# Optimization experiments

Hardware: AMD Instinct MI355X
Metric: run time of the kernel (lower is better)

Reference implementation:

```python
import jax, jax.numpy as jnp
import numpy as np
from functools import reduce

IN_CH = 1; OUT_CH = 16; K = 3; PAD = 1; QDEPTH = 2; WIRES = 4; DIM = 2 ** WIRES

# --- precomputed CNOT permutation matrices (constants) ---
# PennyLane convention: wire 0 is the most significant bit of the basis index.
def _cnot_mat(control, target):
    perm = np.arange(DIM)
    cbit = 1 << (WIRES - 1 - control)
    tbit = 1 << (WIRES - 1 - target)
    flip = (perm & cbit).astype(bool)
    perm = np.where(flip, perm ^ tbit, perm)
    return jnp.asarray(np.eye(DIM, dtype=np.complex64)[perm])

# StronglyEntanglingLayers default ranges: r_l = l % (n_wires - 1) + 1
_CNOTS = [[_cnot_mat(i, (i + (l % (WIRES - 1) + 1)) % WIRES) for i in range(WIRES)]
          for l in range(QDEPTH)]

def _rot(angles):
    # qml.Rot(phi, theta, omega) = RZ(omega) @ RY(theta) @ RZ(phi)
    phi, theta, omega = angles[0], angles[1], angles[2]
    c = jnp.cos(theta / 2); s = jnp.sin(theta / 2)
    return jnp.stack([
        jnp.exp(-0.5j * (phi + omega)) * c, -jnp.exp(0.5j * (phi - omega)) * s,
        jnp.exp(-0.5j * (phi - omega)) * s,  jnp.exp(0.5j * (phi + omega)) * c,
    ]).reshape(2, 2)

def _sel_unitary(weights):
    # Full 16x16 unitary of StronglyEntanglingLayers(weights) -- dim is tiny,
    # so building the dense unitary once and batching patches through it is
    # the efficient form (vs. per-gate contractions over 2.1M state vectors).
    U = jnp.eye(DIM, dtype=jnp.complex64)
    for l in range(QDEPTH):
        layer = reduce(jnp.kron, [_rot(weights[l, i]) for i in range(WIRES)])
        U = layer @ U
        for C in _CNOTS[l]:
            U = C @ U
    return U

def setup_inputs() -> dict:
    key = jax.random.key(0)
    k1, k2 = jax.random.split(key)
    x = jax.random.normal(k1, (32, 1, 256, 256), dtype=jnp.float32)
    weights = jax.random.uniform(k2, (QDEPTH, WIRES, 3), dtype=jnp.float32)
    return {"x": x, "weights": weights}

def reference(x, weights):
    b, c, h_in, w_in = x.shape
    h_out = h_in + 2 * PAD - K + 1
    w_out = w_in + 2 * PAD - K + 1
    # ConstantPad2d with value 0.01
    xp = jnp.pad(x, ((0, 0), (0, 0), (PAD, PAD), (PAD, PAD)), constant_values=0.01)
    # unfold -> (b, c*K*K, h_out, w_out), feature order (c, k0, k1)
    patches = jax.lax.conv_general_dilated_patches(xp, (K, K), (1, 1), 'VALID')
    patches = patches.transpose(0, 2, 3, 1).reshape(b * h_out * w_out, K * K)
    # zero-pad patch vectors from K*K=9 to 2^wires=16, then L2-normalize (eps=1e-12)
    patches = jnp.pad(patches, ((0, 0), (0, DIM - K * K)))
    norm = jnp.linalg.norm(patches, axis=-1, keepdims=True)
    patches = patches / jnp.maximum(norm, 1e-12)
    # Mottonen prep on |0> yields the normalized patch exactly (up to global
    # phase); then apply the entangling-layer unitary and measure probs.
    state = patches.astype(jnp.complex64) @ _sel_unitary(weights).T  # (N, 16)
    probs = jnp.abs(state) ** 2
    out = jnp.clip(probs * (DIM * 0.5), 0.0, 1.0)[:, :OUT_CH]
    return out.reshape(b, h_out, w_out, OUT_CH).transpose(0, 3, 1, 2)
```

## Files before the change

kernel.cpp:

```cpp
#include <hip/hip_runtime.h>
#include <math.h>


#define WIRES 4
#define DIM 16

__device__ inline void rot_entry(float phi, float th, float om, int rb, int cb,
                                 float& er, float& ei) {
    float a = 0.5f * (phi + om);
    float b = 0.5f * (phi - om);
    float cc = cosf(0.5f * th), ss = sinf(0.5f * th);
    if (rb == 0 && cb == 0) { er = cc * cosf(a); ei = -cc * sinf(a); }
    else if (rb == 0 && cb == 1) { er = -ss * cosf(b); ei = -ss * sinf(b); }
    else if (rb == 1 && cb == 0) { er = ss * cosf(b); ei = -ss * sinf(b); }
    else { er = cc * cosf(a); ei = cc * sinf(a); }
}

__device__ inline void layer_elem(const float* __restrict__ w, int l, int r,
                                  int c, float& pr, float& pi) {
    pr = 1.f; pi = 0.f;
    #pragma unroll
    for (int i = 0; i < WIRES; ++i) {
        const float* wi = w + (l * WIRES + i) * 3;
        float er, ei;
        int rb = (r >> (3 - i)) & 1, cb = (c >> (3 - i)) & 1;
        rot_entry(wi[0], wi[1], wi[2], rb, cb, er, ei);
        float nr = pr * er - pi * ei;
        float ni = pr * ei + pi * er;
        pr = nr; pi = ni;
    }
}

__device__ inline int cnot_src(int r, int range) {
    int src = r;
    #pragma unroll
    for (int i = WIRES - 1; i >= 0; --i) {
        int control = i, target = (i + range) & 3;
        int cbit = 1 << (3 - control), tbit = 1 << (3 - target);
        if (src & cbit) src ^= tbit;
    }
    return src;
}

__global__ __launch_bounds__(256) void build_unitary(
        const float* __restrict__ w, float* __restrict__ uout) {
    __shared__ float Lr[DIM][DIM], Li[DIM][DIM];
    __shared__ float Ur[DIM][DIM], Ui[DIM][DIM];
    __shared__ float Tr[DIM][DIM], Ti[DIM][DIM];
    int t = threadIdx.x;
    int r = t >> 4, c = t & 15;

    float lr, li;
    layer_elem(w, 0, r, c, lr, li);
    Lr[r][c] = lr; Li[r][c] = li;
    __syncthreads();
    int s0 = cnot_src(r, 1);
    Ur[r][c] = Lr[s0][c]; Ui[r][c] = Li[s0][c];
    __syncthreads();

    layer_elem(w, 1, r, c, lr, li);
    Lr[r][c] = lr; Li[r][c] = li;
    __syncthreads();
    float ar = 0.f, ai = 0.f;
    #pragma unroll
    for (int m = 0; m < DIM; ++m) {
        float xr = Lr[r][m], xi = Li[r][m];
        float yr = Ur[m][c], yi = Ui[m][c];
        ar += xr * yr - xi * yi;
        ai += xr * yi + xi * yr;
    }
    Tr[r][c] = ar; Ti[r][c] = ai;
    __syncthreads();
    int s1 = cnot_src(r, 2);
    uout[r * DIM + c]       = Tr[s1][c];
    uout[256 + r * DIM + c] = Ti[s1][c];
}

#define H 256
#define W 256
#define NB 32
#define OUTC 16
#define RPB 4
#define LDSW 264

__global__ __launch_bounds__(256) void qconv_kernel(
        const float* __restrict__ x, const float* __restrict__ u,
        float* __restrict__ out) {
    __shared__ float sUr[OUTC][9];
    __shared__ float sUi[OUTC][9];
    __shared__ float rows[RPB + 2][LDSW];

    int t = threadIdx.x;
    int blk = blockIdx.x;
    int b  = blk >> 6;
    int i0 = (blk & 63) * RPB;

    if (t < OUTC * 9) {
        int k = t / 9, m = t % 9;
        sUr[k][m] = u[k * DIM + m];
        sUi[k][m] = u[256 + k * DIM + m];
    }

    const float* xb = x + (size_t)b * H * W;
    #pragma unroll
    for (int r = 0; r < RPB + 2; ++r) {
        int gr = i0 + r - 1;
        for (int c = t; c < W + 2; c += 256) {
            int j = c - 1;
            float v = 0.01f;
            if ((unsigned)gr < (unsigned)H && (unsigned)j < (unsigned)W)
                v = xb[gr * W + j];
            rows[r][c] = v;
        }
    }
    __syncthreads();

    int lr = t >> 6;
    int j0 = (t & 63) * 4;

    float win[3][6];
    #pragma unroll
    for (int di = 0; di < 3; ++di) {
        float4 a  = *(const float4*)&rows[lr + di][j0];
        float2 bb = *(const float2*)&rows[lr + di][j0 + 4];
        win[di][0] = a.x;  win[di][1] = a.y;  win[di][2] = a.z;
        win[di][3] = a.w;  win[di][4] = bb.x; win[di][5] = bb.y;
    }

    float factor[4];
    #pragma unroll
    for (int q = 0; q < 4; ++q) {
        float n2 = 0.f;
        #pragma unroll
        for (int di = 0; di < 3; ++di)
            #pragma unroll
            for (int dj = 0; dj < 3; ++dj) {
                float v = win[di][q + dj];
                n2 = fmaf(v, v, n2);
            }
        factor[q] = 8.0f / fmaxf(n2, 1e-24f);
    }

    int i = i0 + lr;
    float* ob = out + ((size_t)b * OUTC * H + i) * W + j0;

    #pragma unroll 4
    for (int k = 0; k < OUTC; ++k) {
        float cr[9], ci[9];
        #pragma unroll
        for (int m = 0; m < 9; ++m) { cr[m] = sUr[k][m]; ci[m] = sUi[k][m]; }
        float4 o;
        float* op = &o.x;
        #pragma unroll
        for (int q = 0; q < 4; ++q) {
            float sr = 0.f, si = 0.f;
            #pragma unroll
            for (int di = 0; di < 3; ++di)
                #pragma unroll
                for (int dj = 0; dj < 3; ++dj) {
                    float v = win[di][q + dj];
                    int m = di * 3 + dj;
                    sr = fmaf(cr[m], v, sr);
                    si = fmaf(ci[m], v, si);
                }
            op[q] = fminf(factor[q] * (sr * sr + si * si), 1.0f);
        }
        *(float4*)(ob + (size_t)k * H * W) = o;
    }
}

extern "C" void kernel_launch(void* const* d_in, const int* in_sizes, int n_in,
                              void* d_out, int out_size, void* d_ws, size_t ws_size,
                              hipStream_t stream) {
    const float* x = (const float*)d_in[0];
    const float* w = (const float*)d_in[1];
    float* out = (float*)d_out;
    float* uws = (float*)d_ws;

    build_unitary<<<1, 256, 0, stream>>>(w, uws);
    qconv_kernel<<<NB * (H / RPB), 256, 0, stream>>>(x, uws, out);
}
```

Measured before the change: 179.0 us.

## Process 8 rows and 8 pixels per thread with nontemporal output stores

Each block now covers 8 output rows instead of 4, and each thread computes 8 consecutive pixels instead of 4. This halves the block count and cuts the halo-row reload overhead per output. Output is written with nontemporal vector stores so the large streaming output does not pollute the cache. The division in the normalization factor is replaced with the hardware reciprocal builtin. In exchange, register pressure per thread rises and fewer blocks are available to hide latency.

```diff
diff --git a/kernel.cpp b/kernel.cpp
--- a/kernel.cpp
+++ b/kernel.cpp
@@ -4,6 +4,8 @@
 
 #define WIRES 4
 #define DIM 16
+
+typedef float v4f __attribute__((ext_vector_type(4)));
 
 __device__ inline void rot_entry(float phi, float th, float om, int rb, int cb,
                                  float& er, float& ei) {
@@ -80,7 +82,8 @@
 #define W 256
 #define NB 32
 #define OUTC 16
-#define RPB 4
+#define RPB 8
+#define PXT 8
 #define LDSW 264
 
 __global__ __launch_bounds__(256) void qconv_kernel(
@@ -92,8 +95,8 @@
 
     int t = threadIdx.x;
     int blk = blockIdx.x;
-    int b  = blk >> 6;
-    int i0 = (blk & 63) * RPB;
+    int b  = blk >> 5;
+    int i0 = (blk & 31) * RPB;
 
     if (t < OUTC * 9) {
         int k = t / 9, m = t % 9;
@@ -115,21 +118,23 @@
     }
     __syncthreads();
 
-    int lr = t >> 6;
-    int j0 = (t & 63) * 4;
+    int lr = t >> 5;
+    int j0 = (t & 31) * PXT;
 
-    float win[3][6];
+    float win[3][PXT + 2];
     #pragma unroll
     for (int di = 0; di < 3; ++di) {
-        float4 a  = *(const float4*)&rows[lr + di][j0];
-        float2 bb = *(const float2*)&rows[lr + di][j0 + 4];
-        win[di][0] = a.x;  win[di][1] = a.y;  win[di][2] = a.z;
-        win[di][3] = a.w;  win[di][4] = bb.x; win[di][5] = bb.y;
+        float4 a0 = *(const float4*)&rows[lr + di][j0];
+        float4 a1 = *(const float4*)&rows[lr + di][j0 + 4];
+        float2 a2 = *(const float2*)&rows[lr + di][j0 + 8];
+        win[di][0] = a0.x; win[di][1] = a0.y; win[di][2] = a0.z; win[di][3] = a0.w;
+        win[di][4] = a1.x; win[di][5] = a1.y; win[di][6] = a1.z; win[di][7] = a1.w;
+        win[di][8] = a2.x; win[di][9] = a2.y;
     }
 
-    float factor[4];
+    float factor[PXT];
     #pragma unroll
-    for (int q = 0; q < 4; ++q) {
+    for (int q = 0; q < PXT; ++q) {
         float n2 = 0.f;
         #pragma unroll
         for (int di = 0; di < 3; ++di)
@@ -138,21 +143,20 @@
                 float v = win[di][q + dj];
                 n2 = fmaf(v, v, n2);
             }
-        factor[q] = 8.0f / fmaxf(n2, 1e-24f);
+        factor[q] = 8.0f * __builtin_amdgcn_rcpf(fmaxf(n2, 1e-24f));
     }
 
     int i = i0 + lr;
     float* ob = out + ((size_t)b * OUTC * H + i) * W + j0;
 
-    #pragma unroll 4
+    #pragma unroll 2
     for (int k = 0; k < OUTC; ++k) {
         float cr[9], ci[9];
         #pragma unroll
         for (int m = 0; m < 9; ++m) { cr[m] = sUr[k][m]; ci[m] = sUi[k][m]; }
-        float4 o;
-        float* op = &o.x;
+        float o[PXT];
         #pragma unroll
-        for (int q = 0; q < 4; ++q) {
+        for (int q = 0; q < PXT; ++q) {
             float sr = 0.f, si = 0.f;
             #pragma unroll
             for (int di = 0; di < 3; ++di)
@@ -163,9 +167,13 @@
                     sr = fmaf(cr[m], v, sr);
                     si = fmaf(ci[m], v, si);
                 }
-            op[q] = fminf(factor[q] * (sr * sr + si * si), 1.0f);
+            o[q] = fminf(factor[q] * (sr * sr + si * si), 1.0f);
         }
-        *(float4*)(ob + (size_t)k * H * W) = o;
+        v4f o0 = { o[0], o[1], o[2], o[3] };
+        v4f o1 = { o[4], o[5], o[6], o[7] };
+        float* dst = ob + (size_t)k * H * W;
+        __builtin_nontemporal_store(o0, (v4f*)dst);
+        __builtin_nontemporal_store(o1, (v4f*)(dst + 4));
     }
 }
 
```

New measurement: 211.7 us. +18.3%, slower.
